# Kernel optimization log

Measured on AMD Instinct MI355X. Metric: run time of the kernel, lower is better.

The kernel has to match this reference:

```python
import jax, jax.numpy as jnp
import numpy as np

N = 100000
E = 1600000
C_IN = 32
C_OUT = 64
B = 4
VOXEL_SIZE = 0.0625
GRID_LO, GRID_HI = 0.0, 1.0
VOX = int((GRID_HI - GRID_LO) / VOXEL_SIZE)  # 16
R_CORR = GRID_HI - GRID_LO  # r_correction = max(grid_scale) - min(grid_scale) = 1


def setup_inputs() -> dict:
    key = jax.random.key(0)
    k1, k2, k3, k4, k5, k6 = jax.random.split(key, 6)
    x = jax.random.normal(k1, (N, C_IN), dtype=jnp.float32)
    edge_index = jax.random.randint(k2, (2, E), 0, N, dtype=jnp.int32)
    pos = jax.random.uniform(k3, (N, 2), dtype=jnp.float32)
    batch = jnp.sort(jax.random.randint(k4, (N,), 0, B, dtype=jnp.int32))
    W = jax.random.normal(k5, (C_OUT, 4 * C_IN), dtype=jnp.float32) / np.sqrt(4 * C_IN)
    b = jax.random.normal(k6, (C_OUT,), dtype=jnp.float32) * 0.01
    return {"x": x, "edge_index": edge_index, "pos": pos, "batch": batch, "W": W, "b": b}


def dpo_conv(x, edge_index, pos, W, b):
    row, col = edge_index[0], edge_index[1]  # j = source, i = target (PyG default flow)
    pos_i, pos_j = pos[col], pos[row]        # [E, 2]
    v_i, v_j = x[col], x[row]                # [E, C_IN]
    diff = pos_i - pos_j                     # [E, 2]
    r2 = jnp.sum(diff * diff, axis=1, keepdims=True)  # [E, 1]
    w = diff * R_CORR / (r2 + 0.01)          # [E, 2] -> columns are diff_x, diff_y
    v_diff = v_i - v_j                       # [E, C_IN]
    # message f: [E, 3*C_IN]
    f = jnp.concatenate([v_diff * w[:, 0:1], v_diff * w[:, 1:2], v_j], axis=1)
    # scatter-mean into target nodes i = col
    summed = jax.ops.segment_sum(f, col, num_segments=N)            # [N, 3*C_IN]
    cnt = jax.ops.segment_sum(jnp.ones((E, 1), f.dtype), col, num_segments=N)
    prop = summed / jnp.maximum(cnt, 1.0)
    prop = jnp.concatenate([prop, x], axis=1)  # [N, 4*C_IN]
    return prop @ W.T + b


def reference(x, edge_index, pos, batch, W, b):
    h = jax.nn.relu(dpo_conv(x, edge_index, pos, W, b))  # [N, C_OUT]
    # voxel_grid: per-graph voxel cluster ids, then max_pool per cluster (dense grid)
    vox = jnp.clip(jnp.floor((pos - GRID_LO) / VOXEL_SIZE).astype(jnp.int32), 0, VOX - 1)
    cluster = batch * (VOX * VOX) + vox[:, 1] * VOX + vox[:, 0]     # [N]
    n_clusters = B * VOX * VOX
    pooled_x = jax.ops.segment_max(h, cluster, num_segments=n_clusters)  # [B*V^2, C_OUT]
    pooled_x = jnp.where(jnp.isfinite(pooled_x), pooled_x, 0.0)          # empty voxels -> 0
    pos_sum = jax.ops.segment_sum(pos, cluster, num_segments=n_clusters)
    node_cnt = jax.ops.segment_sum(jnp.ones((N, 1), pos.dtype), cluster, num_segments=n_clusters)
    pooled_pos = pos_sum / jnp.maximum(node_cnt, 1.0)                    # mean pos per voxel
    return pooled_x, pooled_pos, pos, batch
```

## Files before the change

kernel.cpp:

```cpp
#include <hip/hip_runtime.h>
#include <hip/hip_fp16.h>

#define NN 100000
#define NE 1600000
#define NCLUST 1024
#define OUT_POOLED_POS 65536
#define OUT_POS        67584
#define OUT_BATCH      267584
#define ZROW ((unsigned)NN)

static __device__ __forceinline__ float2 h2f(unsigned int u)
{
    __half2 h = *reinterpret_cast<__half2*>(&u);
    return __half22float2(h);
}

__global__ __launch_bounds__(256) void cvt_kernel(const float4* __restrict__ x4,
                                                  uint2* __restrict__ xh2)
{
    int t = blockIdx.x * 256 + threadIdx.x;
    if (t >= NN * 8) return;
    float4 v = x4[t];
    __half2 lo = __floats2half2_rn(v.x, v.y);
    __half2 hi = __floats2half2_rn(v.z, v.w);
    uint2 o;
    o.x = *reinterpret_cast<unsigned int*>(&lo);
    o.y = *reinterpret_cast<unsigned int*>(&hi);
    xh2[t] = o;
}

__global__ __launch_bounds__(256) void fill_kernel(const int* __restrict__ ei,
                                                   const float2* __restrict__ pos2,
                                                   int* __restrict__ wp,
                                                   uint2* __restrict__ csr64,
                                                   int cap)
{
    int t = blockIdx.x * 256 + threadIdx.x;
    int e0 = t * 4;
    if (e0 + 3 < NE) {
        int4 r = *(const int4*)(ei + e0);
        int4 c = *(const int4*)(ei + NE + e0);
        int rr[4] = {r.x, r.y, r.z, r.w};
        int cc[4] = {c.x, c.y, c.z, c.w};
        #pragma unroll
        for (int u = 0; u < 4; ++u) {
            int row = rr[u], col = cc[u];
            float2 pi = pos2[col], pj = pos2[row];
            float dx = pi.x - pj.x, dy = pi.y - pj.y;
            float inv = __builtin_amdgcn_rcpf(dx * dx + dy * dy + 0.01f);
            __half2 h2 = __floats2half2_rn(dx * inv, dy * inv);
            unsigned int wbits = *reinterpret_cast<unsigned int*>(&h2);
            int s = atomicAdd(&wp[col], 1);
            if (s < cap) csr64[(size_t)col * cap + s] = make_uint2((unsigned)row, wbits);
        }
    } else {
        for (int e = e0; e < NE; ++e) {
            int row = ei[e], col = ei[NE + e];
            float2 pi = pos2[col], pj = pos2[row];
            float dx = pi.x - pj.x, dy = pi.y - pj.y;
            float inv = __builtin_amdgcn_rcpf(dx * dx + dy * dy + 0.01f);
            __half2 h2 = __floats2half2_rn(dx * inv, dy * inv);
            unsigned int wbits = *reinterpret_cast<unsigned int*>(&h2);
            int s = atomicAdd(&wp[col], 1);
            if (s < cap) csr64[(size_t)col * cap + s] = make_uint2((unsigned)row, wbits);
        }
    }
}

__global__ __launch_bounds__(1024, 4) void fused_kernel(
    const float2* __restrict__ xf2,
    const unsigned int* __restrict__ xh32,
    const float2* __restrict__ pos2,
    const int* __restrict__ batch,
    const float4* __restrict__ W4,
    const float* __restrict__ bv,
    const int* __restrict__ wp,
    const uint2* __restrict__ csr64,
    int cap,
    float* __restrict__ out,
    float* __restrict__ pos_sum,
    float* __restrict__ node_cnt)
{
    __shared__ float4 Wt4[32 * 64];
    __shared__ float  bs[64];
    __shared__ float4 prop4[16][4][32];

    {
        int oc0 = threadIdx.x & 63;
        int k0  = threadIdx.x >> 6;
        Wt4[k0 * 64 + oc0]        = W4[oc0 * 32 + k0];
        Wt4[(k0 + 16) * 64 + oc0] = W4[oc0 * 32 + k0 + 16];
        if (threadIdx.x < 64) bs[threadIdx.x] = bv[threadIdx.x];
    }
    __syncthreads();

    const int wid  = threadIdx.x >> 6;
    const int lane = threadIdx.x & 63;
    const int q  = lane >> 4;
    const int s  = lane & 15;
    const int oc = lane;
    const int nwaves = gridDim.x * 16;
    const uint2 ZE = make_uint2(ZROW, 0u);

    for (int wg = blockIdx.x * 16 + wid; wg * 4 < NN; wg += nwaves) {
        int n = wg * 4 + q;
        bool act = (n < NN);
        int nn = act ? n : 0;

        int cnt = wp[nn];
        int deg = act ? min(cnt, cap) : 0;
        float2 vi = xf2[(size_t)nn * 16 + s];
        const uint2* bk = csr64 + (size_t)nn * cap;

        int md = deg;
        md = max(md, __shfl_xor(md, 16));
        md = max(md, __shfl_xor(md, 32));

        float a0x = 0.f, a0y = 0.f;
        float a1x = 0.f, a1y = 0.f;
        float a2x = 0.f, a2y = 0.f;

        uint2    En[8];
        unsigned Xc[8], Wc[8];
        unsigned Xn[8], Wn[8];

        #pragma unroll
        for (int u = 0; u < 8; ++u) En[u] = (u < deg) ? bk[u] : ZE;
        #pragma unroll
        for (int u = 0; u < 8; ++u) {
            Xc[u] = xh32[(size_t)En[u].x * 16 + s];
            Wc[u] = En[u].y;
        }
        #pragma unroll
        for (int u = 0; u < 8; ++u) En[u] = (8 + u < deg) ? bk[8 + u] : ZE;

        int iters = (md + 7) >> 3;
        for (int it = 0; it < iters; ++it) {
            if (it + 1 < iters) {
                #pragma unroll
                for (int u = 0; u < 8; ++u) {
                    Xn[u] = xh32[(size_t)En[u].x * 16 + s];
                    Wn[u] = En[u].y;
                }
            }
            if (it + 2 < iters) {
                int b2 = (it + 2) * 8;
                #pragma unroll
                for (int u = 0; u < 8; ++u)
                    En[u] = (b2 + u < deg) ? bk[b2 + u] : ZE;
            }
            #pragma unroll
            for (int u = 0; u < 8; ++u) {
                float2 w = h2f(Wc[u]), v = h2f(Xc[u]);
                float vdx = vi.x - v.x, vdy = vi.y - v.y;
                a0x += vdx * w.x; a0y += vdy * w.x;
                a1x += vdx * w.y; a1y += vdy * w.y;
                a2x += v.x;       a2y += v.y;
            }
            #pragma unroll
            for (int u = 0; u < 8; ++u) { Xc[u] = Xn[u]; Wc[u] = Wn[u]; }
        }

        float invd = 1.0f / fmaxf((float)cnt, 1.0f);
        if (act) {
            float2* pw = (float2*)&prop4[wid][q][0];
            pw[s]      = make_float2(a0x * invd, a0y * invd);
            pw[16 + s] = make_float2(a1x * invd, a1y * invd);
            pw[32 + s] = make_float2(a2x * invd, a2y * invd);
            pw[48 + s] = vi;
        }
        asm volatile("s_waitcnt lgkmcnt(0)" ::: "memory");

        float bb = bs[oc];
        float acc0 = bb, acc1 = bb, acc2 = bb, acc3 = bb;
        #pragma unroll 8
        for (int k4 = 0; k4 < 32; ++k4) {
            float4 w   = Wt4[k4 * 64 + oc];
            float4 pp0 = prop4[wid][0][k4];
            float4 pp1 = prop4[wid][1][k4];
            float4 pp2 = prop4[wid][2][k4];
            float4 pp3 = prop4[wid][3][k4];
            acc0 += w.x*pp0.x + w.y*pp0.y + w.z*pp0.z + w.w*pp0.w;
            acc1 += w.x*pp1.x + w.y*pp1.y + w.z*pp1.z + w.w*pp1.w;
            acc2 += w.x*pp2.x + w.y*pp2.y + w.z*pp2.z + w.w*pp2.w;
            acc3 += w.x*pp3.x + w.y*pp3.y + w.z*pp3.z + w.w*pp3.w;
        }

        float accq[4] = {acc0, acc1, acc2, acc3};
        #pragma unroll
        for (int qq = 0; qq < 4; ++qq) {
            int n2 = wg * 4 + qq;
            if (n2 < NN) {
                float h = fmaxf(accq[qq], 0.0f);
                float2 pp = pos2[n2];
                int b = batch[n2];
                int vx = min(max((int)floorf(pp.x * 16.0f), 0), 15);
                int vy = min(max((int)floorf(pp.y * 16.0f), 0), 15);
                int cl = b * 256 + vy * 16 + vx;
                unsigned int* tgt = (unsigned int*)(out + (size_t)cl * 64 + oc);
                unsigned int prev = *tgt;
                unsigned int cur  = __float_as_uint(h);
                if (cur > prev) atomicMax(tgt, cur);
                if (oc == qq) {
                    *(float2*)(out + OUT_POS + 2 * (size_t)n2) = pp;
                    out[OUT_BATCH + n2] = (float)b;
                    atomicAdd(pos_sum + 2 * cl,     pp.x);
                    atomicAdd(pos_sum + 2 * cl + 1, pp.y);
                    atomicAdd(node_cnt + cl, 1.0f);
                }
            }
        }
        asm volatile("s_waitcnt lgkmcnt(0)" ::: "memory");
    }
}

__global__ void finalize_kernel(const float* __restrict__ pos_sum,
                                const float* __restrict__ node_cnt,
                                float* __restrict__ out_pooled_pos)
{
    int c = blockIdx.x * blockDim.x + threadIdx.x;
    if (c >= NCLUST) return;
    float inv = 1.0f / fmaxf(node_cnt[c], 1.0f);
    out_pooled_pos[2 * c]     = pos_sum[2 * c] * inv;
    out_pooled_pos[2 * c + 1] = pos_sum[2 * c + 1] * inv;
}

extern "C" void kernel_launch(void* const* d_in, const int* in_sizes, int n_in,
                              void* d_out, int out_size, void* d_ws, size_t ws_size,
                              hipStream_t stream)
{
    const float* x     = (const float*)d_in[0];
    const int*   ei    = (const int*)d_in[1];
    const float* pos   = (const float*)d_in[2];
    const int*   batch = (const int*)d_in[3];
    const float* W     = (const float*)d_in[4];
    const float* bvec  = (const float*)d_in[5];
    float* out = (float*)d_out;

    size_t fixed = (size_t)NN * 4 + (size_t)(NN + 1) * 8 * 8 + 3 * NCLUST * 4;
    int cap = 40;
    if (ws_size < fixed + (size_t)NN * cap * 8) {
        cap = (int)((ws_size - fixed) / ((size_t)NN * 8));
        if (cap > 40) cap = 40;
    }

    int* wp = (int*)d_ws;
    uint2* csr64 = (uint2*)(wp + NN);
    uint2* xh2 = csr64 + (size_t)NN * cap;
    float* pos_sum  = (float*)(xh2 + (size_t)(NN + 1) * 8);
    float* node_cnt = pos_sum + 2 * NCLUST;

    hipMemsetAsync(wp, 0, NN * sizeof(int), stream);
    hipMemsetAsync(xh2 + (size_t)NN * 8, 0, 64, stream);
    hipMemsetAsync(pos_sum, 0, 3 * NCLUST * sizeof(float), stream);
    hipMemsetAsync(d_out, 0, (size_t)NCLUST * 64 * sizeof(float), stream);

    cvt_kernel<<<(NN * 8 + 255) / 256, 256, 0, stream>>>((const float4*)x, xh2);

    fill_kernel<<<(NE / 4 + 255) / 256, 256, 0, stream>>>(
        ei, (const float2*)pos, wp, csr64, cap);

    fused_kernel<<<512, 1024, 0, stream>>>(
        (const float2*)x, (const unsigned int*)xh2, (const float2*)pos, batch,
        (const float4*)W, bvec, wp, csr64, cap, out, pos_sum, node_cnt);

    finalize_kernel<<<(NCLUST + 255) / 256, 256, 0, stream>>>(
        pos_sum, node_cnt, out + NCLUST * 64);
}
```

Before: 282.9 us.

## Store only source index in CSR and recompute edge weights in fused kernel

The fill kernel no longer gathers positions or computes the per-edge geometric weight; it writes only the 4-byte source index into the bucketed CSR instead of an 8-byte index+half2 pair. The fused kernel now gathers pos[j] for each neighbor and recomputes the weight in fp32, uses int4 vector loads of the CSR bucket, and narrows the unroll from 8 to 4 with a one-stage prefetch. This halves CSR write/read traffic and removes random pos gathers from the atomic fill pass, at the cost of an extra scattered pos load per edge in the hot aggregation loop. The launch bound min-blocks hint also rises from 4 to 8.

Result: slower. 410.9 us (+45.3%).

```diff
diff --git a/kernel.cpp b/kernel.cpp
--- a/kernel.cpp
+++ b/kernel.cpp
@@ -30,9 +30,8 @@
 }
 
 __global__ __launch_bounds__(256) void fill_kernel(const int* __restrict__ ei,
-                                                   const float2* __restrict__ pos2,
                                                    int* __restrict__ wp,
-                                                   uint2* __restrict__ csr64,
+                                                   int* __restrict__ csr,
                                                    int cap)
 {
     int t = blockIdx.x * 256 + threadIdx.x;
@@ -40,34 +39,21 @@
     if (e0 + 3 < NE) {
         int4 r = *(const int4*)(ei + e0);
         int4 c = *(const int4*)(ei + NE + e0);
-        int rr[4] = {r.x, r.y, r.z, r.w};
-        int cc[4] = {c.x, c.y, c.z, c.w};
-        #pragma unroll
-        for (int u = 0; u < 4; ++u) {
-            int row = rr[u], col = cc[u];
-            float2 pi = pos2[col], pj = pos2[row];
-            float dx = pi.x - pj.x, dy = pi.y - pj.y;
-            float inv = __builtin_amdgcn_rcpf(dx * dx + dy * dy + 0.01f);
-            __half2 h2 = __floats2half2_rn(dx * inv, dy * inv);
-            unsigned int wbits = *reinterpret_cast<unsigned int*>(&h2);
-            int s = atomicAdd(&wp[col], 1);
-            if (s < cap) csr64[(size_t)col * cap + s] = make_uint2((unsigned)row, wbits);
-        }
+        int s;
+        s = atomicAdd(&wp[c.x], 1); if (s < cap) csr[(size_t)c.x * cap + s] = r.x;
+        s = atomicAdd(&wp[c.y], 1); if (s < cap) csr[(size_t)c.y * cap + s] = r.y;
+        s = atomicAdd(&wp[c.z], 1); if (s < cap) csr[(size_t)c.z * cap + s] = r.z;
+        s = atomicAdd(&wp[c.w], 1); if (s < cap) csr[(size_t)c.w * cap + s] = r.w;
     } else {
         for (int e = e0; e < NE; ++e) {
-            int row = ei[e], col = ei[NE + e];
-            float2 pi = pos2[col], pj = pos2[row];
-            float dx = pi.x - pj.x, dy = pi.y - pj.y;
-            float inv = __builtin_amdgcn_rcpf(dx * dx + dy * dy + 0.01f);
-            __half2 h2 = __floats2half2_rn(dx * inv, dy * inv);
-            unsigned int wbits = *reinterpret_cast<unsigned int*>(&h2);
-            int s = atomicAdd(&wp[col], 1);
-            if (s < cap) csr64[(size_t)col * cap + s] = make_uint2((unsigned)row, wbits);
-        }
-    }
-}
-
-__global__ __launch_bounds__(1024, 4) void fused_kernel(
+            int c = ei[NE + e];
+            int s = atomicAdd(&wp[c], 1);
+            if (s < cap) csr[(size_t)c * cap + s] = ei[e];
+        }
+    }
+}
+
+__global__ __launch_bounds__(1024, 8) void fused_kernel(
     const float2* __restrict__ xf2,
     const unsigned int* __restrict__ xh32,
     const float2* __restrict__ pos2,
@@ -75,7 +61,7 @@
     const float4* __restrict__ W4,
     const float* __restrict__ bv,
     const int* __restrict__ wp,
-    const uint2* __restrict__ csr64,
+    const int* __restrict__ csr,
     int cap,
     float* __restrict__ out,
     float* __restrict__ pos_sum,
@@ -100,7 +86,6 @@
     const int s  = lane & 15;
     const int oc = lane;
     const int nwaves = gridDim.x * 16;
-    const uint2 ZE = make_uint2(ZROW, 0u);
 
     for (int wg = blockIdx.x * 16 + wid; wg * 4 < NN; wg += nwaves) {
         int n = wg * 4 + q;
@@ -110,7 +95,8 @@
         int cnt = wp[nn];
         int deg = act ? min(cnt, cap) : 0;
         float2 vi = xf2[(size_t)nn * 16 + s];
-        const uint2* bk = csr64 + (size_t)nn * cap;
+        float2 pi = pos2[nn];
+        const int* bk = csr + (size_t)nn * cap;
 
         int md = deg;
         md = max(md, __shfl_xor(md, 16));
@@ -120,45 +106,55 @@
         float a1x = 0.f, a1y = 0.f;
         float a2x = 0.f, a2y = 0.f;
 
-        uint2    En[8];
-        unsigned Xc[8], Wc[8];
-        unsigned Xn[8], Wn[8];
-
+        int      J[4];
+        float    M[4];
+        unsigned X[4];
+        float2   PJ[4];
+        int      Jn[4];
+        float    Mn[4];
+
+        {
+            int4 e = *(const int4*)(bk);
+            J[0] = (0 < deg) ? e.x : (int)ZROW; M[0] = (0 < deg) ? 1.f : 0.f;
+            J[1] = (1 < deg) ? e.y : (int)ZROW; M[1] = (1 < deg) ? 1.f : 0.f;
+            J[2] = (2 < deg) ? e.z : (int)ZROW; M[2] = (2 < deg) ? 1.f : 0.f;
+            J[3] = (3 < deg) ? e.w : (int)ZROW; M[3] = (3 < deg) ? 1.f : 0.f;
+        }
         #pragma unroll
-        for (int u = 0; u < 8; ++u) En[u] = (u < deg) ? bk[u] : ZE;
-        #pragma unroll
-        for (int u = 0; u < 8; ++u) {
-            Xc[u] = xh32[(size_t)En[u].x * 16 + s];
-            Wc[u] = En[u].y;
-        }
-        #pragma unroll
-        for (int u = 0; u < 8; ++u) En[u] = (8 + u < deg) ? bk[8 + u] : ZE;
-
-        int iters = (md + 7) >> 3;
+        for (int u = 0; u < 4; ++u) {
+            X[u]  = xh32[(size_t)J[u] * 16 + s];
+            PJ[u] = pos2[min(J[u], NN - 1)];
+        }
+
+        int iters = (md + 3) >> 2;
         for (int it = 0; it < iters; ++it) {
             if (it + 1 < iters) {
+                int b = (it + 1) * 4;
+                int4 e = *(const int4*)(bk + b);
+                Jn[0] = (b     < deg) ? e.x : (int)ZROW; Mn[0] = (b     < deg) ? 1.f : 0.f;
+                Jn[1] = (b + 1 < deg) ? e.y : (int)ZROW; Mn[1] = (b + 1 < deg) ? 1.f : 0.f;
+                Jn[2] = (b + 2 < deg) ? e.z : (int)ZROW; Mn[2] = (b + 2 < deg) ? 1.f : 0.f;
+                Jn[3] = (b + 3 < deg) ? e.w : (int)ZROW; Mn[3] = (b + 3 < deg) ? 1.f : 0.f;
+            }
+            #pragma unroll
+            for (int u = 0; u < 4; ++u) {
+                float dx = pi.x - PJ[u].x, dy = pi.y - PJ[u].y;
+                float inv = __builtin_amdgcn_rcpf(dx * dx + dy * dy + 0.01f) * M[u];
+                float wx = dx * inv, wy = dy * inv;
+                float2 v = h2f(X[u]);
+                float vdx = vi.x - v.x, vdy = vi.y - v.y;
+                a0x += vdx * wx; a0y += vdy * wx;
+                a1x += vdx * wy; a1y += vdy * wy;
+                a2x += v.x;      a2y += v.y;
+            }
+            if (it + 1 < iters) {
                 #pragma unroll
-                for (int u = 0; u < 8; ++u) {
-                    Xn[u] = xh32[(size_t)En[u].x * 16 + s];
-                    Wn[u] = En[u].y;
+                for (int u = 0; u < 4; ++u) {
+                    J[u] = Jn[u]; M[u] = Mn[u];
+                    X[u]  = xh32[(size_t)J[u] * 16 + s];
+                    PJ[u] = pos2[min(J[u], NN - 1)];
                 }
             }
-            if (it + 2 < iters) {
-                int b2 = (it + 2) * 8;
-                #pragma unroll
-                for (int u = 0; u < 8; ++u)
-                    En[u] = (b2 + u < deg) ? bk[b2 + u] : ZE;
-            }
-            #pragma unroll
-            for (int u = 0; u < 8; ++u) {
-                float2 w = h2f(Wc[u]), v = h2f(Xc[u]);
-                float vdx = vi.x - v.x, vdy = vi.y - v.y;
-                a0x += vdx * w.x; a0y += vdy * w.x;
-                a1x += vdx * w.y; a1y += vdy * w.y;
-                a2x += v.x;       a2y += v.y;
-            }
-            #pragma unroll
-            for (int u = 0; u < 8; ++u) { Xc[u] = Xn[u]; Wc[u] = Wn[u]; }
         }
 
         float invd = 1.0f / fmaxf((float)cnt, 1.0f);
@@ -239,14 +235,14 @@
 
     size_t fixed = (size_t)NN * 4 + (size_t)(NN + 1) * 8 * 8 + 3 * NCLUST * 4;
     int cap = 40;
-    if (ws_size < fixed + (size_t)NN * cap * 8) {
-        cap = (int)((ws_size - fixed) / ((size_t)NN * 8));
+    if (ws_size < fixed + (size_t)NN * cap * 4) {
+        cap = (int)((ws_size - fixed) / ((size_t)NN * 4)) & ~3;
         if (cap > 40) cap = 40;
     }
 
     int* wp = (int*)d_ws;
-    uint2* csr64 = (uint2*)(wp + NN);
-    uint2* xh2 = csr64 + (size_t)NN * cap;
+    int* csr = wp + NN;
+    uint2* xh2 = (uint2*)(csr + (size_t)NN * cap);
     float* pos_sum  = (float*)(xh2 + (size_t)(NN + 1) * 8);
     float* node_cnt = pos_sum + 2 * NCLUST;
 
@@ -257,12 +253,11 @@
 
     cvt_kernel<<<(NN * 8 + 255) / 256, 256, 0, stream>>>((const float4*)x, xh2);
 
-    fill_kernel<<<(NE / 4 + 255) / 256, 256, 0, stream>>>(
-        ei, (const float2*)pos, wp, csr64, cap);
+    fill_kernel<<<(NE / 4 + 255) / 256, 256, 0, stream>>>(ei, wp, csr, cap);
 
     fused_kernel<<<512, 1024, 0, stream>>>(
         (const float2*)x, (const unsigned int*)xh2, (const float2*)pos, batch,
-        (const float4*)W, bvec, wp, csr64, cap, out, pos_sum, node_cnt);
+        (const float4*)W, bvec, wp, csr, cap, out, pos_sum, node_cnt);
 
     finalize_kernel<<<(NCLUST + 255) / 256, 256, 0, stream>>>(
         pos_sum, node_cnt, out + NCLUST * 64);
```
